# Kernel tuning notes

Hardware: AMD Instinct MI355X
Metric: run time of the kernel (lower is better)

## Reference

```python
import jax, jax.numpy as jnp
import numpy as np

ALPHA_MIN = float(np.exp(-1.0 / 5.0))   # 0.8187
ALPHA_MAX = float(np.exp(-1.0 / 25.0))  # 0.9608
THRESHOLD = 1.0


def setup_inputs() -> dict:
    key = jax.random.key(0)
    k_x, k_w, k_a, k_u, k_s = jax.random.split(key, 5)
    B, T, I, H = 64, 1000, 1024, 1024
    x = jax.random.normal(k_x, (B, T, I), dtype=jnp.float32)
    # nn.Linear default init ~ U(-1/sqrt(I), 1/sqrt(I)); gaussian of similar scale is fine
    W = jax.random.normal(k_w, (H, I), dtype=jnp.float32) / np.sqrt(I)
    alpha = jax.random.uniform(k_a, (H,), dtype=jnp.float32,
                               minval=ALPHA_MIN, maxval=ALPHA_MAX)
    # original uses torch.rand for initial membrane potential / spikes
    u0 = jax.random.uniform(k_u, (B, H), dtype=jnp.float32)
    s0 = jax.random.uniform(k_s, (B, H), dtype=jnp.float32)
    return {"x": x, "W": W, "alpha": alpha, "u0": u0, "s0": s0}


def reference(x, W, alpha, u0, s0):
    # Input projection: Wx[b,t,h] = sum_i x[b,t,i] * W[h,i]
    Wx = jnp.einsum('bti,hi->bth', x, W)
    a = jnp.clip(alpha, ALPHA_MIN, ALPHA_MAX)  # [H]

    def step(carry, wx_t):
        ut, st = carry                              # each [B, H]
        ut = a * (ut - st) + (1.0 - a) * wx_t       # leaky integrate with reset
        st = (ut - THRESHOLD > 0).astype(ut.dtype)  # hard spike (boxcar surrogate in bwd)
        return (ut, st), st

    # scan over time: Wx -> [T, B, H]
    _, s = jax.lax.scan(step, (u0, s0), jnp.swapaxes(Wx, 0, 1))
    return jnp.swapaxes(s, 0, 1)  # [B, T, H]
```

## Files before the change

kernel.cpp:

```cpp
#include <hip/hip_runtime.h>


#define TM 128
#define TN 64
#define MTK 16
#define VTK 8
#define LDA 130
#define LDB 66

typedef double v4d __attribute__((ext_vector_type(4)));

__global__ __launch_bounds__(256) void transpose_w(
    const float* __restrict__ W, double* __restrict__ WdT)
{
    __shared__ float t[32][33];
    const int k0 = blockIdx.x * 32;
    const int n0 = blockIdx.y * 32;
    const int tx = threadIdx.x & 31;
    const int ty = threadIdx.x >> 5;
    #pragma unroll
    for (int i = 0; i < 4; i++)
        t[ty + 8 * i][tx] = W[(size_t)(n0 + ty + 8 * i) * 1024 + k0 + tx];
    __syncthreads();
    #pragma unroll
    for (int i = 0; i < 4; i++)
        WdT[(size_t)(k0 + ty + 8 * i) * 1024 + n0 + tx] = (double)t[tx][ty + 8 * i];
}

__global__ __launch_bounds__(64) void probe_mfma_layout(unsigned int* __restrict__ flag)
{
    __shared__ double Am[16][4];
    __shared__ double Bm[4][16];
    const int l = threadIdx.x;
    Am[l & 15][l >> 4] = (double)(1 + (l & 15) + 16 * (l >> 4));
    Bm[l >> 4][l & 15] = 1.0 + 0.5 * (double)((l >> 4) + 4 * (l & 15));
    __syncthreads();
    const v4d z = {0.0, 0.0, 0.0, 0.0};
    const double a0 = Am[l & 15][l >> 4];
    const double b0 = Bm[l >> 4][l & 15];
    const double a1 = Am[l >> 2][l & 3];
    const double b1 = Bm[l & 3][l >> 2];
    const v4d d0 = __builtin_amdgcn_mfma_f64_16x16x4f64(a0, b0, z, 0, 0, 0);
    const v4d d1 = __builtin_amdgcn_mfma_f64_16x16x4f64(a1, b1, z, 0, 0, 0);
    int ok[8];
    #pragma unroll
    for (int c = 0; c < 8; c++) ok[c] = 1;
    #pragma unroll
    for (int q = 0; q < 4; q++) {
        const int iD[4] = {4 * (l >> 4) + q, l & 15, (l >> 4) + 4 * q, l & 15};
        const int jD[4] = {l & 15, 4 * (l >> 4) + q, l & 15, (l >> 4) + 4 * q};
        #pragma unroll
        for (int dm = 0; dm < 4; dm++) {
            double ref = 0.0;
            #pragma unroll
            for (int k = 0; k < 4; k++) ref += Am[iD[dm]][k] * Bm[k][jD[dm]];
            if (d0[q] != ref) ok[dm] = 0;
            if (d1[q] != ref) ok[4 + dm] = 0;
        }
    }
    unsigned int f = 255u;
    for (int c = 7; c >= 0; --c)
        if (__all(ok[c])) f = (unsigned int)c;
    if (l == 0) *flag = f;
}

__global__ __launch_bounds__(256, 3) void gemm_f64_mfma(
    const float* __restrict__ A,
    const double* __restrict__ WdT,
    double* __restrict__ C, int M, int N, int K,
    const unsigned int* __restrict__ flag)
{
    const unsigned int f = *flag;
    if (f - 1u > 6u) return;

    __shared__ double As[2][MTK][LDA];
    __shared__ double Bs[2][MTK][LDB];

    const int tid  = threadIdx.x;
    const int lane = tid & 63;
    const int l16  = lane & 15;
    const int kq4  = lane >> 4;
    const int wid  = tid >> 6;
    const int wr   = wid >> 1;
    const int wc   = wid & 1;

    const int imap = (int)(f >> 2);
    const int dmap = (int)(f & 3u);
    const int rowl = imap ? (lane >> 2) : l16;
    const int kl   = imap ? (lane & 3)  : kq4;
    int rloc, rstep, cloc, cstep;
    switch (dmap) {
        case 0:  rloc = 4 * kq4; rstep = 1; cloc = l16;     cstep = 0; break;
        case 1:  rloc = l16;     rstep = 0; cloc = 4 * kq4; cstep = 1; break;
        case 2:  rloc = kq4;     rstep = 4; cloc = l16;     cstep = 0; break;
        default: rloc = l16;     rstep = 0; cloc = kq4;     cstep = 4; break;
    }

    const int nb0 = blockIdx.x * TN;
    const int tm  = blockIdx.y * TM;

    const int rA  = tid >> 1;
    const int kA  = (tid & 1) * 4;
    const int kkB = tid >> 4;
    const int cBl = (tid & 15) * 4;

    v4d acc[4][2];
    #pragma unroll
    for (int i = 0; i < 4; i++)
        #pragma unroll
        for (int j = 0; j < 2; j++)
            acc[i][j] = (v4d)0.0;

    const int ar = min(tm + rA, M - 1);
    const float* Apg = A + (size_t)ar * K;
    const double* Bpg = WdT + (size_t)kkB * N + nb0 + cBl;

    struct StReg { float4 a0, a1; double2 b0, b1; };
    auto issue = [&](int s) {
        StReg t;
        const int k0 = s * MTK;
        t.a0 = *(const float4*)(Apg + k0 + kA);
        t.a1 = *(const float4*)(Apg + k0 + kA + 8);
        const double* wp = Bpg + (size_t)k0 * N;
        t.b0 = *(const double2*)(wp);
        t.b1 = *(const double2*)(wp + 2);
        return t;
    };
    auto commit = [&](int buf, const StReg& t) {
        As[buf][kA + 0][rA] = (double)t.a0.x;
        As[buf][kA + 1][rA] = (double)t.a0.y;
        As[buf][kA + 2][rA] = (double)t.a0.z;
        As[buf][kA + 3][rA] = (double)t.a0.w;
        As[buf][kA + 8][rA] = (double)t.a1.x;
        As[buf][kA + 9][rA] = (double)t.a1.y;
        As[buf][kA + 10][rA] = (double)t.a1.z;
        As[buf][kA + 11][rA] = (double)t.a1.w;
        Bs[buf][kkB][cBl + 0] = t.b0.x;
        Bs[buf][kkB][cBl + 1] = t.b0.y;
        Bs[buf][kkB][cBl + 2] = t.b1.x;
        Bs[buf][kkB][cBl + 3] = t.b1.y;
    };

    const int mw = wr * 64;
    const int nw = wc * 32;
    auto compute_tile = [&](int p) {
        #pragma unroll
        for (int ks = 0; ks < 4; ++ks) {
            const int kk = ks * 4 + kl;
            double av[4], bv[2];
            #pragma unroll
            for (int i = 0; i < 4; i++) av[i] = As[p][kk][mw + i * 16 + rowl];
            #pragma unroll
            for (int j = 0; j < 2; j++) bv[j] = Bs[p][kk][nw + j * 16 + rowl];
            #pragma unroll
            for (int i = 0; i < 4; i++)
                #pragma unroll
                for (int j = 0; j < 2; j++)
                    acc[i][j] = __builtin_amdgcn_mfma_f64_16x16x4f64(
                        av[i], bv[j], acc[i][j], 0, 0, 0);
        }
    };

    commit(0, issue(0));
    __syncthreads();

    const int NR = K / MTK;
    for (int s = 0; s < NR - 1; ++s) {
        const int p = s & 1;
        StReg t = issue(s + 1);
        compute_tile(p);
        commit(1 - p, t);
        __syncthreads();
    }
    compute_tile((NR - 1) & 1);

    const int mwR = tm + mw;
    const int nwC = nb0 + nw;
    #pragma unroll
    for (int i = 0; i < 4; i++) {
        #pragma unroll
        for (int q = 0; q < 4; q++) {
            const int row = mwR + i * 16 + rloc + q * rstep;
            if (row < M) {
                double* Cr = C + (size_t)row * N + nwC + cloc + q * cstep;
                Cr[0]  = acc[i][0][q];
                Cr[16] = acc[i][1][q];
            }
        }
    }
}

__global__ __launch_bounds__(256, 3) void gemm_f64_sgpr(
    const float* __restrict__ A,
    const double* __restrict__ WdT,
    double* __restrict__ C, int M, int N, int K,
    const unsigned int* __restrict__ flag)
{
    {
        const unsigned int f = *flag;
        if (f - 1u <= 6u) return;
    }
    __shared__ double As[2][VTK][LDA];

    const int tid  = threadIdx.x;
    const int lane = tid & 63;
    const int nb = __builtin_amdgcn_readfirstlane(blockIdx.x * TN + (tid >> 6) * 16);
    const int tm = blockIdx.y * TM;

    const int kq = (tid & 1) * 4;
    const int r  = tid >> 1;

    double acc0[16], acc1[16];
    #pragma unroll
    for (int j = 0; j < 16; j++) { acc0[j] = 0.0; acc1[j] = 0.0; }

    const int ar = min(tm + r, M - 1);
    const float* Ap = A + (size_t)ar * K + kq;

    {
        const float4 a0 = *(const float4*)(Ap);
        As[0][kq + 0][r] = (double)a0.x; As[0][kq + 1][r] = (double)a0.y;
        As[0][kq + 2][r] = (double)a0.z; As[0][kq + 3][r] = (double)a0.w;
    }
    __syncthreads();

    auto compute_tile = [&](int p, int k0) {
        #pragma unroll
        for (int kk = 0; kk < VTK; kk++) {
            const double* wr = WdT + (size_t)(k0 + kk) * N + nb;
            const double2 a = *(const double2*)&As[p][kk][2 * lane];
            #pragma unroll
            for (int j = 0; j < 16; j++) {
                const double wj = wr[j];
                acc0[j] = fma(a.x, wj, acc0[j]);
                acc1[j] = fma(a.y, wj, acc1[j]);
            }
        }
    };

    const int NS = K / VTK;
    for (int s = 0; s < NS - 1; ++s) {
        const int p = s & 1;
        {
            const float4 a0 = *(const float4*)(Ap + (size_t)(s + 1) * VTK);
            const int q = 1 - p;
            As[q][kq + 0][r] = (double)a0.x; As[q][kq + 1][r] = (double)a0.y;
            As[q][kq + 2][r] = (double)a0.z; As[q][kq + 3][r] = (double)a0.w;
        }
        compute_tile(p, s * VTK);
        __syncthreads();
    }
    compute_tile((NS - 1) & 1, (NS - 1) * VTK);

    const int m0 = tm + 2 * lane;
    if (m0 < M) {
        double* Cr = C + (size_t)m0 * N + nb;
        #pragma unroll
        for (int j = 0; j < 8; j++)
            *(double2*)&Cr[2 * j] = double2{acc0[2 * j], acc0[2 * j + 1]};
    }
    if (m0 + 1 < M) {
        double* Cr = C + (size_t)(m0 + 1) * N + nb;
        #pragma unroll
        for (int j = 0; j < 8; j++)
            *(double2*)&Cr[2 * j] = double2{acc1[2 * j], acc1[2 * j + 1]};
    }
}

__global__ __launch_bounds__(256) void lif_scan_kernel(
    const double* __restrict__ Wx,
    const float* __restrict__ alpha,
    const float* __restrict__ u0,
    const float* __restrict__ s0,
    float* __restrict__ out,
    int b0, int T, int H)
{
    const int idx = blockIdx.x * blockDim.x + threadIdx.x;
    const int h  = idx & 1023;
    const int bl = idx >> 10;
    const int b  = b0 + bl;

    const double AMIN = 0.8187307530779818;
    const double AMAX = 0.9607894391523232;
    double a = (double)alpha[h];
    a = fmin(fmax(a, AMIN), AMAX);
    const double oma = 1.0 - a;

    double u = (double)u0[(size_t)b * H + h];
    double s = (double)s0[(size_t)b * H + h];

    const double* wp = Wx + (size_t)bl * T * H + h;
    float* op = out + (size_t)b * T * H + h;

    double v[8];
    #pragma unroll
    for (int p = 0; p < 8; p++) v[p] = wp[(size_t)p * H];

    for (int t0 = 0; t0 < T; t0 += 8) {
        double nv[8];
        const bool more = (t0 + 8) < T;
        const double* wn = wp + (size_t)(t0 + 8) * H;
        #pragma unroll
        for (int p = 0; p < 8; p++) nv[p] = more ? wn[(size_t)p * H] : 0.0;

        #pragma unroll
        for (int p = 0; p < 8; p++) {
            u = a * (u - s) + oma * v[p];
            s = (u - 1.0 > 0.0) ? 1.0 : 0.0;
            op[(size_t)(t0 + p) * H] = (float)s;
        }
        #pragma unroll
        for (int p = 0; p < 8; p++) v[p] = nv[p];
    }
}

extern "C" void kernel_launch(void* const* d_in, const int* in_sizes, int n_in,
                              void* d_out, int out_size, void* d_ws, size_t ws_size,
                              hipStream_t stream) {
    const float* x     = (const float*)d_in[0];
    const float* W     = (const float*)d_in[1];
    const float* alpha = (const float*)d_in[2];
    const float* u0    = (const float*)d_in[3];
    const float* s0    = (const float*)d_in[4];
    float* out = (float*)d_out;
    const int Bt = 64, T = 1000, I = 1024, H = 1024;

    double* wdT = (double*)d_ws;
    const size_t wdT_bytes = (size_t)I * H * sizeof(double);
    const size_t flag_off = (ws_size - 256) & ~(size_t)255;
    unsigned int* flag = (unsigned int*)((char*)d_ws + flag_off);
    double* wx = (double*)((char*)d_ws + wdT_bytes);
    const size_t avail = (flag_off > wdT_bytes) ? flag_off - wdT_bytes : 0;

    const size_t per_batch = (size_t)T * H * sizeof(double);
    int Bc = 1;
    {
        const int cands[7] = {64, 32, 16, 8, 4, 2, 1};
        for (int c = 0; c < 7; c++) {
            if ((size_t)cands[c] * per_batch <= avail) { Bc = cands[c]; break; }
        }
    }

    transpose_w<<<dim3(1024 / 32, 1024 / 32), 256, 0, stream>>>(W, wdT);
    probe_mfma_layout<<<1, 64, 0, stream>>>(flag);

    for (int b0 = 0; b0 < Bt; b0 += Bc) {
        const int M = Bc * T;
        dim3 grid(H / TN, (M + TM - 1) / TM);
        gemm_f64_mfma<<<grid, 256, 0, stream>>>(
            x + (size_t)b0 * T * I, wdT, wx, M, H, I, flag);
        gemm_f64_sgpr<<<grid, 256, 0, stream>>>(
            x + (size_t)b0 * T * I, wdT, wx, M, H, I, flag);
        lif_scan_kernel<<<(Bc * H) / 256, 256, 0, stream>>>(
            wx, alpha, u0, s0, out, b0, T, H);
    }
}
```

Measured before the change: 2.438 ms.

## Load B operand directly from global into registers, drop B shared tile

The f64 MFMA GEMM no longer stages the W^T tile through shared memory. Each lane now loads its B fragments straight from global memory into registers, prefetched one k-step ahead. Dropping the Bs shared buffer and its LDS traffic is meant to free LDS, and launch bounds are raised to 4 blocks per CU to improve occupancy. The cost is redundant global and L2 reads of B across warps, plus extra register pressure for the prefetched B fragments.

```diff
diff --git a/kernel.cpp b/kernel.cpp
--- a/kernel.cpp
+++ b/kernel.cpp
@@ -6,7 +6,6 @@
 #define MTK 16
 #define VTK 8
 #define LDA 130
-#define LDB 66
 
 typedef double v4d __attribute__((ext_vector_type(4)));
 
@@ -64,7 +63,7 @@
     if (l == 0) *flag = f;
 }
 
-__global__ __launch_bounds__(256, 3) void gemm_f64_mfma(
+__global__ __launch_bounds__(256, 4) void gemm_f64_mfma(
     const float* __restrict__ A,
     const double* __restrict__ WdT,
     double* __restrict__ C, int M, int N, int K,
@@ -74,7 +73,6 @@
     if (f - 1u > 6u) return;
 
     __shared__ double As[2][MTK][LDA];
-    __shared__ double Bs[2][MTK][LDB];
 
     const int tid  = threadIdx.x;
     const int lane = tid & 63;
@@ -101,8 +99,6 @@
 
     const int rA  = tid >> 1;
     const int kA  = (tid & 1) * 4;
-    const int kkB = tid >> 4;
-    const int cBl = (tid & 15) * 4;
 
     v4d acc[4][2];
     #pragma unroll
@@ -113,20 +109,19 @@
 
     const int ar = min(tm + rA, M - 1);
     const float* Apg = A + (size_t)ar * K;
-    const double* Bpg = WdT + (size_t)kkB * N + nb0 + cBl;
-
-    struct StReg { float4 a0, a1; double2 b0, b1; };
-    auto issue = [&](int s) {
-        StReg t;
+    const int nw = wc * 32;
+    const int mw = wr * 64;
+    const double* Bln = WdT + (size_t)kl * N + nb0 + nw + rowl;
+
+    struct AReg { float4 a0, a1; };
+    auto issueA = [&](int s) {
+        AReg t;
         const int k0 = s * MTK;
         t.a0 = *(const float4*)(Apg + k0 + kA);
         t.a1 = *(const float4*)(Apg + k0 + kA + 8);
-        const double* wp = Bpg + (size_t)k0 * N;
-        t.b0 = *(const double2*)(wp);
-        t.b1 = *(const double2*)(wp + 2);
         return t;
     };
-    auto commit = [&](int buf, const StReg& t) {
+    auto commitA = [&](int buf, const AReg& t) {
         As[buf][kA + 0][rA] = (double)t.a0.x;
         As[buf][kA + 1][rA] = (double)t.a0.y;
         As[buf][kA + 2][rA] = (double)t.a0.z;
@@ -135,44 +130,52 @@
         As[buf][kA + 9][rA] = (double)t.a1.y;
         As[buf][kA + 10][rA] = (double)t.a1.z;
         As[buf][kA + 11][rA] = (double)t.a1.w;
-        Bs[buf][kkB][cBl + 0] = t.b0.x;
-        Bs[buf][kkB][cBl + 1] = t.b0.y;
-        Bs[buf][kkB][cBl + 2] = t.b1.x;
-        Bs[buf][kkB][cBl + 3] = t.b1.y;
-    };
-
-    const int mw = wr * 64;
-    const int nw = wc * 32;
-    auto compute_tile = [&](int p) {
+    };
+
+    struct BReg { double b[4][2]; };
+    auto loadB = [&](int s) {
+        BReg r;
+        const int k0 = s * MTK;
+        #pragma unroll
+        for (int ks = 0; ks < 4; ++ks) {
+            const double* bp = Bln + (size_t)(k0 + ks * 4) * N;
+            r.b[ks][0] = bp[0];
+            r.b[ks][1] = bp[16];
+        }
+        return r;
+    };
+
+    auto compute_tile = [&](int p, const BReg& br) {
         #pragma unroll
         for (int ks = 0; ks < 4; ++ks) {
             const int kk = ks * 4 + kl;
-            double av[4], bv[2];
+            double av[4];
             #pragma unroll
             for (int i = 0; i < 4; i++) av[i] = As[p][kk][mw + i * 16 + rowl];
-            #pragma unroll
-            for (int j = 0; j < 2; j++) bv[j] = Bs[p][kk][nw + j * 16 + rowl];
             #pragma unroll
             for (int i = 0; i < 4; i++)
                 #pragma unroll
                 for (int j = 0; j < 2; j++)
                     acc[i][j] = __builtin_amdgcn_mfma_f64_16x16x4f64(
-                        av[i], bv[j], acc[i][j], 0, 0, 0);
-        }
-    };
-
-    commit(0, issue(0));
+                        av[i], br.b[ks][j], acc[i][j], 0, 0, 0);
+        }
+    };
+
+    BReg bcur = loadB(0);
+    commitA(0, issueA(0));
     __syncthreads();
 
     const int NR = K / MTK;
     for (int s = 0; s < NR - 1; ++s) {
         const int p = s & 1;
-        StReg t = issue(s + 1);
-        compute_tile(p);
-        commit(1 - p, t);
+        AReg a = issueA(s + 1);
+        BReg bnext = loadB(s + 1);
+        compute_tile(p, bcur);
+        commitA(1 - p, a);
+        bcur = bnext;
         __syncthreads();
     }
-    compute_tile((NR - 1) & 1);
+    compute_tile((NR - 1) & 1, bcur);
 
     const int mwR = tm + mw;
     const int nwC = nb0 + nw;
```

Result: slower. 2.502 ms (+2.6%).
